# Performance work log

Hardware: AMD Instinct MI355X
Metric: run time of the kernel (lower is better)

## Reference

```python
import jax, jax.numpy as jnp
import numpy as np

N = 50000      # nodes
E = 1_600_000  # edges
FN = 8         # num_node_features
FE = 8         # num_edge_features
H = 16         # hidden_layers[0]
IH = 10        # intra_hidden


def _lin(k, i, o):
    return (jax.random.normal(k, (i, o), dtype=jnp.float32) / np.sqrt(i)).astype(jnp.float32)


def setup_inputs() -> dict:
    key = jax.random.key(0)
    ks = jax.random.split(key, 16)
    d = {}
    d["x"] = jax.random.normal(ks[0], (N, FN), dtype=jnp.float32)
    d["edge_attr"] = jax.random.normal(ks[1], (E, FE), dtype=jnp.float32)
    d["edge_index"] = jax.random.randint(ks[2], (2, E), 0, N)
    # NNConv 0: in=FN, out=H; edge-nn: FE -> IH -> FN*H
    d["c0_w1"] = _lin(ks[3], FE, IH);  d["c0_b1"] = jnp.zeros((IH,), jnp.float32)
    d["c0_w2"] = _lin(ks[4], IH, FN * H); d["c0_b2"] = jnp.zeros((FN * H,), jnp.float32)
    d["c0_root"] = _lin(ks[5], FN, H); d["c0_bias"] = jnp.zeros((H,), jnp.float32)
    # NNConv 1: in=H, out=IH; edge-nn: FE -> IH -> H*IH
    d["c1_w1"] = _lin(ks[6], FE, IH);  d["c1_b1"] = jnp.zeros((IH,), jnp.float32)
    d["c1_w2"] = _lin(ks[7], IH, H * IH); d["c1_b2"] = jnp.zeros((H * IH,), jnp.float32)
    d["c1_root"] = _lin(ks[8], H, IH); d["c1_bias"] = jnp.zeros((IH,), jnp.float32)
    # edge predictor: (FE+IH) -> IH -> 1
    d["ep_w1"] = _lin(ks[9], FE + IH, IH); d["ep_b1"] = jnp.zeros((IH,), jnp.float32)
    d["ep_w2"] = _lin(ks[10], IH, 1); d["ep_b2"] = jnp.zeros((1,), jnp.float32)
    return d


def _nnconv(x, edge_index, edge_attr, w1, b1, w2, b2, root, bias, in_ch, out_ch):
    """PyG NNConv (aggr='add', root_weight=True): per-edge weight from edge MLP,
    gather source features, per-edge matvec, scatter-add to targets, plus root term."""
    src, dst = edge_index[0], edge_index[1]
    w = jax.nn.relu(edge_attr @ w1 + b1) @ w2 + b2        # [E, in*out]
    w = w.reshape(-1, in_ch, out_ch)                       # [E, in, out]
    msg = jnp.einsum('ei,eio->eo', x[src], w)              # [E, out]
    agg = jax.ops.segment_sum(msg, dst, num_segments=x.shape[0])  # [N, out]
    return agg + x @ root + bias


def reference(x, edge_attr, edge_index,
              c0_w1, c0_b1, c0_w2, c0_b2, c0_root, c0_bias,
              c1_w1, c1_b1, c1_w2, c1_b2, c1_root, c1_bias,
              ep_w1, ep_b1, ep_w2, ep_b2):
    h = jax.nn.relu(_nnconv(x, edge_index, edge_attr,
                            c0_w1, c0_b1, c0_w2, c0_b2, c0_root, c0_bias, FN, H))
    h = jax.nn.relu(_nnconv(h, edge_index, edge_attr,
                            c1_w1, c1_b1, c1_w2, c1_b2, c1_root, c1_bias, H, IH))
    feat = jnp.concatenate([edge_attr, h[edge_index[0]]], axis=1)  # [E, FE+IH]
    scores = jax.nn.relu(feat @ ep_w1 + ep_b1) @ ep_w2 + ep_b2     # [E, 1]
    return scores.squeeze(-1)
```

## Files before the change

### kernel.cpp

```cpp
#include <hip/hip_runtime.h>

#define N_NODES 50000
#define E_EDGES 1600000
#define FN 8
#define FE 8
#define HID 16
#define IH 10
#define NB_SCAN 196

#define I_CNT   0
#define I_OFF   50048
#define I_RANK  100096
#define I_BSUM  1700096
#define I_BBASE 1700352
#define I_TOTAL 1700608
#define F_H     0
#define F_H2    800000
#define F_MSG   1300000
#define F_TOTAL 26900000
#define WS_NEED ((size_t)I_TOTAL*4 + (size_t)F_TOTAL*4)

__global__ __launch_bounds__(256) void count_rank_k(
    const int* __restrict__ ei, int* __restrict__ cnt, int* __restrict__ rank)
{
    int e = blockIdx.x * 256 + threadIdx.x;
    if (e >= E_EDGES) return;
    int dst = ei[E_EDGES + e];
    rank[e] = atomicAdd(&cnt[dst], 1);
}

__global__ __launch_bounds__(256) void blocksum_k(
    const int* __restrict__ cnt, int* __restrict__ bsum)
{
    __shared__ int sh[256];
    int t = threadIdx.x;
    int idx = blockIdx.x * 256 + t;
    sh[t] = (idx < N_NODES) ? cnt[idx] : 0;
    __syncthreads();
#pragma unroll
    for (int d = 128; d > 0; d >>= 1) {
        if (t < d) sh[t] += sh[t + d];
        __syncthreads();
    }
    if (t == 0) bsum[blockIdx.x] = sh[0];
}

__global__ __launch_bounds__(256) void scan_bsums_k(
    const int* __restrict__ bsum, int* __restrict__ bbase)
{
    __shared__ int sh[256];
    int t = threadIdx.x;
    int v = (t < NB_SCAN) ? bsum[t] : 0;
    sh[t] = v;
    __syncthreads();
#pragma unroll
    for (int d = 1; d < 256; d <<= 1) {
        int u = (t >= d) ? sh[t - d] : 0;
        __syncthreads();
        sh[t] += u;
        __syncthreads();
    }
    if (t < NB_SCAN) bbase[t] = sh[t] - v;
}

__global__ __launch_bounds__(256) void offsets_k(
    const int* __restrict__ cnt, const int* __restrict__ bbase,
    int* __restrict__ offset)
{
    __shared__ int sh[256];
    int t = threadIdx.x;
    int b = blockIdx.x;
    int idx = b * 256 + t;
    int v = (idx < N_NODES) ? cnt[idx] : 0;
    sh[t] = v;
    __syncthreads();
#pragma unroll
    for (int d = 1; d < 256; d <<= 1) {
        int u = (t >= d) ? sh[t - d] : 0;
        __syncthreads();
        sh[t] += u;
        __syncthreads();
    }
    int incl = sh[t];
    int base = bbase[b];
    if (idx < N_NODES) offset[idx] = base + incl - v;
    if (idx == N_NODES - 1) offset[N_NODES] = base + incl;
}

__device__ __forceinline__ void load8(const float* __restrict__ p, float v[8]) {
    const float4* q = reinterpret_cast<const float4*>(p);
    float4 a = q[0], b = q[1];
    v[0]=a.x; v[1]=a.y; v[2]=a.z; v[3]=a.w;
    v[4]=b.x; v[5]=b.y; v[6]=b.z; v[7]=b.w;
}

__device__ __forceinline__ void edge_mlp(
    const float eav[FE], const float* __restrict__ w1,
    const float* __restrict__ b1, float u[IH])
{
#pragma unroll
    for (int h = 0; h < IH; ++h) {
        float s = b1[h];
#pragma unroll
        for (int k = 0; k < FE; ++k) s = fmaf(eav[k], w1[k*IH + h], s);
        u[h] = fmaxf(s, 0.f);
    }
}

__global__ __launch_bounds__(256) void conv0_scatter_k(
    const float* __restrict__ x, const float* __restrict__ ea,
    const int* __restrict__ ei,
    const float* __restrict__ w1, const float* __restrict__ b1,
    const float* __restrict__ w2, const float* __restrict__ b2,
    const int* __restrict__ offset, const int* __restrict__ rank,
    float* __restrict__ msgbuf)
{
    int e = blockIdx.x * 256 + threadIdx.x;
    if (e >= E_EDGES) return;
    int src = ei[e];
    int dst = ei[E_EDGES + e];

    float eav[FE];
    load8(ea + (size_t)e * FE, eav);
    float u[IH];
    edge_mlp(eav, w1, b1, u);
    float xv[FN];
    load8(x + (size_t)src * FN, xv);

    float msg[HID];
#pragma unroll
    for (int o = 0; o < HID; ++o) msg[o] = 0.f;
#pragma unroll
    for (int i = 0; i < FN; ++i) {
        float xi = xv[i];
#pragma unroll
        for (int o = 0; o < HID; ++o) {
            float t = b2[i*HID + o];
#pragma unroll
            for (int h = 0; h < IH; ++h)
                t = fmaf(u[h], w2[h*(FN*HID) + i*HID + o], t);
            msg[o] = fmaf(xi, t, msg[o]);
        }
    }
    size_t pos = (size_t)(offset[dst] + rank[e]) * HID;
    float4* mp = reinterpret_cast<float4*>(msgbuf + pos);
    mp[0] = make_float4(msg[0],  msg[1],  msg[2],  msg[3]);
    mp[1] = make_float4(msg[4],  msg[5],  msg[6],  msg[7]);
    mp[2] = make_float4(msg[8],  msg[9],  msg[10], msg[11]);
    mp[3] = make_float4(msg[12], msg[13], msg[14], msg[15]);
}

__global__ __launch_bounds__(256) void node0_red_k(
    const float* __restrict__ x, const float* __restrict__ msgbuf,
    const int* __restrict__ offset,
    const float* __restrict__ root, const float* __restrict__ bias,
    float* __restrict__ h)
{
    int idx = blockIdx.x * 256 + threadIdx.x;
    if (idx >= N_NODES * HID) return;
    int n = idx >> 4;
    int o = idx & 15;
    int beg = offset[n], end = offset[n + 1];
    float s = bias[o];
    for (int j = beg; j < end; ++j) s += msgbuf[(size_t)j * HID + o];
    const float* xr = x + (size_t)n * FN;
#pragma unroll
    for (int i = 0; i < FN; ++i) s = fmaf(xr[i], root[i*HID + o], s);
    h[idx] = fmaxf(s, 0.f);
}

__global__ __launch_bounds__(256) void conv1_scatter_k(
    const float* __restrict__ hin, const float* __restrict__ ea,
    const int* __restrict__ ei,
    const float* __restrict__ w1, const float* __restrict__ b1,
    const float* __restrict__ w2, const float* __restrict__ b2,
    const int* __restrict__ offset, const int* __restrict__ rank,
    float* __restrict__ msgbuf)
{
    int e = blockIdx.x * 256 + threadIdx.x;
    if (e >= E_EDGES) return;
    int src = ei[e];
    int dst = ei[E_EDGES + e];

    float eav[FE];
    load8(ea + (size_t)e * FE, eav);
    float u[IH];
    edge_mlp(eav, w1, b1, u);
    float hv[HID];
    {
        const float4* p = reinterpret_cast<const float4*>(hin + (size_t)src * HID);
        float4 a = p[0], b = p[1], c = p[2], d = p[3];
        hv[0]=a.x;  hv[1]=a.y;  hv[2]=a.z;   hv[3]=a.w;
        hv[4]=b.x;  hv[5]=b.y;  hv[6]=b.z;   hv[7]=b.w;
        hv[8]=c.x;  hv[9]=c.y;  hv[10]=c.z;  hv[11]=c.w;
        hv[12]=d.x; hv[13]=d.y; hv[14]=d.z;  hv[15]=d.w;
    }
    float msg[IH];
#pragma unroll
    for (int o = 0; o < IH; ++o) msg[o] = 0.f;
#pragma unroll
    for (int i = 0; i < HID; ++i) {
        float hi = hv[i];
#pragma unroll
        for (int o = 0; o < IH; ++o) {
            float t = b2[i*IH + o];
#pragma unroll
            for (int h = 0; h < IH; ++h)
                t = fmaf(u[h], w2[h*(HID*IH) + i*IH + o], t);
            msg[o] = fmaf(hi, t, msg[o]);
        }
    }
    size_t pos = (size_t)(offset[dst] + rank[e]) * IH;
    float2* mp = reinterpret_cast<float2*>(msgbuf + pos);
    mp[0] = make_float2(msg[0], msg[1]);
    mp[1] = make_float2(msg[2], msg[3]);
    mp[2] = make_float2(msg[4], msg[5]);
    mp[3] = make_float2(msg[6], msg[7]);
    mp[4] = make_float2(msg[8], msg[9]);
}

__global__ __launch_bounds__(256) void node1_red_k(
    const float* __restrict__ hin, const float* __restrict__ msgbuf,
    const int* __restrict__ offset,
    const float* __restrict__ root, const float* __restrict__ bias,
    float* __restrict__ h2)
{
    int idx = blockIdx.x * 256 + threadIdx.x;
    if (idx >= N_NODES * IH) return;
    int n = idx / IH;
    int o = idx - n * IH;
    int beg = offset[n], end = offset[n + 1];
    float s = bias[o];
    for (int j = beg; j < end; ++j) s += msgbuf[(size_t)j * IH + o];
    const float* hr = hin + (size_t)n * HID;
#pragma unroll
    for (int i = 0; i < HID; ++i) s = fmaf(hr[i], root[i*IH + o], s);
    h2[idx] = fmaxf(s, 0.f);
}

__global__ __launch_bounds__(256) void edge_pred_k(
    const float* __restrict__ h2, const float* __restrict__ ea,
    const int* __restrict__ ei,
    const float* __restrict__ w1, const float* __restrict__ b1,
    const float* __restrict__ w2, const float* __restrict__ b2,
    float* __restrict__ out)
{
    int e = blockIdx.x * 256 + threadIdx.x;
    if (e >= E_EDGES) return;
    int src = ei[e];
    float eav[FE];
    load8(ea + (size_t)e * FE, eav);
    float hv[IH];
    {
        const float2* p = reinterpret_cast<const float2*>(h2 + (size_t)src * IH);
        float2 a = p[0], b = p[1], c = p[2], d = p[3], f = p[4];
        hv[0]=a.x; hv[1]=a.y; hv[2]=b.x; hv[3]=b.y; hv[4]=c.x;
        hv[5]=c.y; hv[6]=d.x; hv[7]=d.y; hv[8]=f.x; hv[9]=f.y;
    }
    float score = b2[0];
#pragma unroll
    for (int j = 0; j < IH; ++j) {
        float s = b1[j];
#pragma unroll
        for (int k = 0; k < FE; ++k) s = fmaf(eav[k], w1[k*IH + j], s);
#pragma unroll
        for (int k = 0; k < IH; ++k) s = fmaf(hv[k], w1[(FE + k)*IH + j], s);
        s = fmaxf(s, 0.f);
        score = fmaf(s, w2[j], score);
    }
    out[e] = score;
}

__global__ __launch_bounds__(256) void conv0_edge_k(
    const float* __restrict__ x, const float* __restrict__ ea,
    const int* __restrict__ ei,
    const float* __restrict__ w1, const float* __restrict__ b1,
    const float* __restrict__ w2, const float* __restrict__ b2,
    float* __restrict__ agg)
{
    int e = blockIdx.x * 256 + threadIdx.x;
    if (e >= E_EDGES) return;
    int src = ei[e];
    int dst = ei[E_EDGES + e];
    float eav[FE];
    load8(ea + (size_t)e * FE, eav);
    float u[IH];
    edge_mlp(eav, w1, b1, u);
    float xv[FN];
    load8(x + (size_t)src * FN, xv);
    float msg[HID];
#pragma unroll
    for (int o = 0; o < HID; ++o) msg[o] = 0.f;
#pragma unroll
    for (int i = 0; i < FN; ++i) {
        float xi = xv[i];
#pragma unroll
        for (int o = 0; o < HID; ++o) {
            float t = b2[i*HID + o];
#pragma unroll
            for (int h = 0; h < IH; ++h)
                t = fmaf(u[h], w2[h*(FN*HID) + i*HID + o], t);
            msg[o] = fmaf(xi, t, msg[o]);
        }
    }
    float* ap = agg + (size_t)dst * HID;
#pragma unroll
    for (int o = 0; o < HID; ++o) atomicAdd(ap + o, msg[o]);
}

__global__ __launch_bounds__(256) void node0_k(
    const float* __restrict__ x, const float* __restrict__ agg,
    const float* __restrict__ root, const float* __restrict__ bias,
    float* __restrict__ h)
{
    int idx = blockIdx.x * 256 + threadIdx.x;
    if (idx >= N_NODES * HID) return;
    int n = idx >> 4;
    int o = idx & 15;
    float s = agg[idx] + bias[o];
    const float* xr = x + (size_t)n * FN;
#pragma unroll
    for (int i = 0; i < FN; ++i) s = fmaf(xr[i], root[i*HID + o], s);
    h[idx] = fmaxf(s, 0.f);
}

__global__ __launch_bounds__(256) void conv1_edge_k(
    const float* __restrict__ hin, const float* __restrict__ ea,
    const int* __restrict__ ei,
    const float* __restrict__ w1, const float* __restrict__ b1,
    const float* __restrict__ w2, const float* __restrict__ b2,
    float* __restrict__ agg)
{
    int e = blockIdx.x * 256 + threadIdx.x;
    if (e >= E_EDGES) return;
    int src = ei[e];
    int dst = ei[E_EDGES + e];
    float eav[FE];
    load8(ea + (size_t)e * FE, eav);
    float u[IH];
    edge_mlp(eav, w1, b1, u);
    float hv[HID];
    {
        const float4* p = reinterpret_cast<const float4*>(hin + (size_t)src * HID);
        float4 a = p[0], b = p[1], c = p[2], d = p[3];
        hv[0]=a.x;  hv[1]=a.y;  hv[2]=a.z;   hv[3]=a.w;
        hv[4]=b.x;  hv[5]=b.y;  hv[6]=b.z;   hv[7]=b.w;
        hv[8]=c.x;  hv[9]=c.y;  hv[10]=c.z;  hv[11]=c.w;
        hv[12]=d.x; hv[13]=d.y; hv[14]=d.z;  hv[15]=d.w;
    }
    float msg[IH];
#pragma unroll
    for (int o = 0; o < IH; ++o) msg[o] = 0.f;
#pragma unroll
    for (int i = 0; i < HID; ++i) {
        float hi = hv[i];
#pragma unroll
        for (int o = 0; o < IH; ++o) {
            float t = b2[i*IH + o];
#pragma unroll
            for (int h = 0; h < IH; ++h)
                t = fmaf(u[h], w2[h*(HID*IH) + i*IH + o], t);
            msg[o] = fmaf(hi, t, msg[o]);
        }
    }
    float* ap = agg + (size_t)dst * IH;
#pragma unroll
    for (int o = 0; o < IH; ++o) atomicAdd(ap + o, msg[o]);
}

__global__ __launch_bounds__(256) void node1_k(
    const float* __restrict__ hin, const float* __restrict__ agg,
    const float* __restrict__ root, const float* __restrict__ bias,
    float* __restrict__ h2)
{
    int idx = blockIdx.x * 256 + threadIdx.x;
    if (idx >= N_NODES * IH) return;
    int n = idx / IH;
    int o = idx - n * IH;
    float s = agg[idx] + bias[o];
    const float* hr = hin + (size_t)n * HID;
#pragma unroll
    for (int i = 0; i < HID; ++i) s = fmaf(hr[i], root[i*IH + o], s);
    h2[idx] = fmaxf(s, 0.f);
}

extern "C" void kernel_launch(void* const* d_in, const int* in_sizes, int n_in,
                              void* d_out, int out_size, void* d_ws, size_t ws_size,
                              hipStream_t stream) {
    const float* x       = (const float*)d_in[0];
    const float* ea      = (const float*)d_in[1];
    const int*   ei      = (const int*)  d_in[2];
    const float* c0_w1   = (const float*)d_in[3];
    const float* c0_b1   = (const float*)d_in[4];
    const float* c0_w2   = (const float*)d_in[5];
    const float* c0_b2   = (const float*)d_in[6];
    const float* c0_root = (const float*)d_in[7];
    const float* c0_bias = (const float*)d_in[8];
    const float* c1_w1   = (const float*)d_in[9];
    const float* c1_b1   = (const float*)d_in[10];
    const float* c1_w2   = (const float*)d_in[11];
    const float* c1_b2   = (const float*)d_in[12];
    const float* c1_root = (const float*)d_in[13];
    const float* c1_bias = (const float*)d_in[14];
    const float* ep_w1   = (const float*)d_in[15];
    const float* ep_b1   = (const float*)d_in[16];
    const float* ep_w2   = (const float*)d_in[17];
    const float* ep_b2   = (const float*)d_in[18];
    float* out = (float*)d_out;

    int eb = (E_EDGES + 255) / 256;

    if (ws_size >= WS_NEED) {
        int*   wi     = (int*)d_ws;
        int*   cnt    = wi + I_CNT;
        int*   offset = wi + I_OFF;
        int*   rank   = wi + I_RANK;
        int*   bsum   = wi + I_BSUM;
        int*   bbase  = wi + I_BBASE;
        float* wf     = (float*)(wi + I_TOTAL);
        float* h      = wf + F_H;
        float* h2     = wf + F_H2;
        float* msg    = wf + F_MSG;

        hipMemsetAsync(cnt, 0, N_NODES * sizeof(int), stream);
        count_rank_k<<<eb, 256, 0, stream>>>(ei, cnt, rank);
        blocksum_k<<<NB_SCAN, 256, 0, stream>>>(cnt, bsum);
        scan_bsums_k<<<1, 256, 0, stream>>>(bsum, bbase);
        offsets_k<<<NB_SCAN, 256, 0, stream>>>(cnt, bbase, offset);

        conv0_scatter_k<<<eb, 256, 0, stream>>>(x, ea, ei, c0_w1, c0_b1, c0_w2, c0_b2,
                                                offset, rank, msg);
        node0_red_k<<<(N_NODES*HID + 255)/256, 256, 0, stream>>>(x, msg, offset,
                                                                 c0_root, c0_bias, h);
        conv1_scatter_k<<<eb, 256, 0, stream>>>(h, ea, ei, c1_w1, c1_b1, c1_w2, c1_b2,
                                                offset, rank, msg);
        node1_red_k<<<(N_NODES*IH + 255)/256, 256, 0, stream>>>(h, msg, offset,
                                                                c1_root, c1_bias, h2);
        edge_pred_k<<<eb, 256, 0, stream>>>(h2, ea, ei, ep_w1, ep_b1, ep_w2, ep_b2, out);
    } else {
        float* ws   = (float*)d_ws;
        float* agg0 = ws;
        float* agg1 = ws + 800000;
        float* h    = ws + 1300000;
        float* h2   = ws + 2100000;
        hipMemsetAsync(d_ws, 0, 1300000 * sizeof(float), stream);
        conv0_edge_k<<<eb, 256, 0, stream>>>(x, ea, ei, c0_w1, c0_b1, c0_w2, c0_b2, agg0);
        node0_k<<<(N_NODES*HID + 255)/256, 256, 0, stream>>>(x, agg0, c0_root, c0_bias, h);
        conv1_edge_k<<<eb, 256, 0, stream>>>(h, ea, ei, c1_w1, c1_b1, c1_w2, c1_b2, agg1);
        node1_k<<<(N_NODES*IH + 255)/256, 256, 0, stream>>>(h, agg1, c1_root, c1_bias, h2);
        edge_pred_k<<<eb, 256, 0, stream>>>(h2, ea, ei, ep_w1, ep_b1, ep_w2, ep_b2, out);
    }
}
```

Baseline: 303.3 us.

## Compute NNConv edge messages with bf16 MFMA over outer-product features

Both NNConv message kernels stop evaluating the per-edge weight matrices with scalar FMAs. Each edge now builds a feature row [x, u⊗x] (and [h, u⊗h] for the second layer) in shared memory, and the message comes from one bf16 16x16x32 MFMA GEMM against the reshaped w2/b2 weights. This turns roughly a thousand per-edge scalar FMAs into matrix-core work, at the cost of bf16 rounding, shared-memory staging and scattered single-float stores to the CSR-ordered buffer. Launch bounds are also changed, and the second-layer kernel moves to 128-thread blocks.

```diff
diff --git a/kernel.cpp b/kernel.cpp
--- a/kernel.cpp
+++ b/kernel.cpp
@@ -1,4 +1,5 @@
 #include <hip/hip_runtime.h>
+#include <hip/hip_bf16.h>
 
 #define N_NODES 50000
 #define E_EDGES 1600000
@@ -20,6 +21,15 @@
 #define F_TOTAL 26900000
 #define WS_NEED ((size_t)I_TOTAL*4 + (size_t)F_TOTAL*4)
 
+typedef __attribute__((ext_vector_type(8))) short bf16x8_t;
+typedef __attribute__((ext_vector_type(4))) float f32x4_t;
+
+__device__ __forceinline__ unsigned pkbf(float a, float b) {
+    union { __hip_bfloat162 v; unsigned u; } r;
+    r.v = __hip_bfloat162(__float2bfloat16(a), __float2bfloat16(b));
+    return r.u;
+}
+
 __global__ __launch_bounds__(256) void count_rank_k(
     const int* __restrict__ ei, int* __restrict__ cnt, int* __restrict__ rank)
 {
@@ -107,7 +117,7 @@
     }
 }
 
-__global__ __launch_bounds__(256) void conv0_scatter_k(
+__global__ __launch_bounds__(256, 3) void conv0_mfma_k(
     const float* __restrict__ x, const float* __restrict__ ea,
     const int* __restrict__ ei,
     const float* __restrict__ w1, const float* __restrict__ b1,
@@ -115,10 +125,34 @@
     const int* __restrict__ offset, const int* __restrict__ rank,
     float* __restrict__ msgbuf)
 {
-    int e = blockIdx.x * 256 + threadIdx.x;
-    if (e >= E_EDGES) return;
+    __shared__ alignas(16) unsigned short feat[16 * 1536];
+    __shared__ alignas(16) unsigned short bfrag[3 * 512];
+    __shared__ int posArr[256];
+
+    int t = threadIdx.x;
+    int e = blockIdx.x * 256 + t;
+
+#pragma unroll
+    for (int q = 0; q < 6; ++q) {
+        int fid = t * 6 + q;
+        int l   = (fid >> 3) & 63;
+        int j   = fid & 7;
+        int s   = fid >> 9;
+        int k   = s * 32 + ((l >> 4) << 3) + j;
+        int o   = l & 15;
+        float wv;
+        if (k < 8)        wv = b2[k * HID + o];
+        else if (k < 88)  { int kk = k - 8; wv = w2[(kk >> 3) * (FN*HID) + (kk & 7) * HID + o]; }
+        else              wv = 0.f;
+        union { __hip_bfloat16 h; unsigned short us; } cv;
+        cv.h = __float2bfloat16(wv);
+        bfrag[fid] = cv.us;
+    }
+    __syncthreads();
+
     int src = ei[e];
     int dst = ei[E_EDGES + e];
+    posArr[t] = offset[dst] + rank[e];
 
     float eav[FE];
     load8(ea + (size_t)e * FE, eav);
@@ -127,27 +161,141 @@
     float xv[FN];
     load8(x + (size_t)src * FN, xv);
 
-    float msg[HID];
-#pragma unroll
-    for (int o = 0; o < HID; ++o) msg[o] = 0.f;
-#pragma unroll
-    for (int i = 0; i < FN; ++i) {
-        float xi = xv[i];
-#pragma unroll
-        for (int o = 0; o < HID; ++o) {
-            float t = b2[i*HID + o];
-#pragma unroll
-            for (int h = 0; h < IH; ++h)
-                t = fmaf(u[h], w2[h*(FN*HID) + i*HID + o], t);
-            msg[o] = fmaf(xi, t, msg[o]);
-        }
-    }
-    size_t pos = (size_t)(offset[dst] + rank[e]) * HID;
-    float4* mp = reinterpret_cast<float4*>(msgbuf + pos);
-    mp[0] = make_float4(msg[0],  msg[1],  msg[2],  msg[3]);
-    mp[1] = make_float4(msg[4],  msg[5],  msg[6],  msg[7]);
-    mp[2] = make_float4(msg[8],  msg[9],  msg[10], msg[11]);
-    mp[3] = make_float4(msg[12], msg[13], msg[14], msg[15]);
+    int m = t >> 4, r = t & 15;
+    unsigned* fb = reinterpret_cast<unsigned*>(feat);
+#pragma unroll
+    for (int c = 0; c < 12; ++c) {
+        float v0,v1,v2,v3,v4,v5,v6,v7;
+        if (c == 0)      { v0=xv[0];v1=xv[1];v2=xv[2];v3=xv[3];v4=xv[4];v5=xv[5];v6=xv[6];v7=xv[7]; }
+        else if (c < 11) { float uh = u[c-1];
+                           v0=uh*xv[0];v1=uh*xv[1];v2=uh*xv[2];v3=uh*xv[3];
+                           v4=uh*xv[4];v5=uh*xv[5];v6=uh*xv[6];v7=uh*xv[7]; }
+        else             { v0=v1=v2=v3=v4=v5=v6=v7=0.f; }
+        int base = m*768 + (((c>>2)*64 + (c&3)*16 + r) << 2);
+        fb[base+0] = pkbf(v0,v1);
+        fb[base+1] = pkbf(v2,v3);
+        fb[base+2] = pkbf(v4,v5);
+        fb[base+3] = pkbf(v6,v7);
+    }
+
+    int lane = t & 63, wave = t >> 6;
+    bf16x8_t bfr[3];
+#pragma unroll
+    for (int s = 0; s < 3; ++s)
+        bfr[s] = *reinterpret_cast<const bf16x8_t*>(&bfrag[s*512 + lane*8]);
+
+    int col = lane & 15, rg = lane >> 4;
+#pragma unroll
+    for (int mm = 0; mm < 4; ++mm) {
+        int mt = wave * 4 + mm;
+        f32x4_t acc = {0.f, 0.f, 0.f, 0.f};
+#pragma unroll
+        for (int s = 0; s < 3; ++s) {
+            bf16x8_t af = *reinterpret_cast<const bf16x8_t*>(
+                &feat[mt*1536 + (s*64 + rg*16 + col)*8]);
+            acc = __builtin_amdgcn_mfma_f32_16x16x32_bf16(af, bfr[s], acc, 0, 0, 0);
+        }
+#pragma unroll
+        for (int j = 0; j < 4; ++j) {
+            int row = rg * 4 + j;
+            int pos = posArr[mt*16 + row];
+            msgbuf[(size_t)pos * HID + col] = acc[j];
+        }
+    }
+}
+
+__global__ __launch_bounds__(128, 2) void conv1_mfma_k(
+    const float* __restrict__ hin, const float* __restrict__ ea,
+    const int* __restrict__ ei,
+    const float* __restrict__ w1, const float* __restrict__ b1,
+    const float* __restrict__ w2, const float* __restrict__ b2,
+    const int* __restrict__ offset, const int* __restrict__ rank,
+    float* __restrict__ msgbuf)
+{
+    __shared__ alignas(16) unsigned short feat[8 * 3072];
+    __shared__ alignas(16) unsigned short bfrag[6 * 512];
+    __shared__ int posArr[128];
+
+    int t = threadIdx.x;
+    int e = blockIdx.x * 128 + t;
+
+#pragma unroll
+    for (int q = 0; q < 24; ++q) {
+        int fid = t * 24 + q;
+        int l   = (fid >> 3) & 63;
+        int j   = fid & 7;
+        int s   = fid >> 9;
+        int k   = s * 32 + ((l >> 4) << 3) + j;
+        int o   = l & 15;
+        float wv = 0.f;
+        if (o < IH) {
+            if (k < 16)        wv = b2[k * IH + o];
+            else if (k < 176)  { int kk = k - 16; wv = w2[(kk >> 4) * (HID*IH) + (kk & 15) * IH + o]; }
+        }
+        union { __hip_bfloat16 h; unsigned short us; } cv;
+        cv.h = __float2bfloat16(wv);
+        bfrag[fid] = cv.us;
+    }
+    __syncthreads();
+
+    int src = ei[e];
+    int dst = ei[E_EDGES + e];
+    posArr[t] = offset[dst] + rank[e];
+
+    float eav[FE];
+    load8(ea + (size_t)e * FE, eav);
+    float u[IH];
+    edge_mlp(eav, w1, b1, u);
+    float hv[HID];
+    load8(hin + (size_t)src * HID,     hv);
+    load8(hin + (size_t)src * HID + 8, hv + 8);
+
+    int m = t >> 4, r = t & 15;
+    unsigned* fb = reinterpret_cast<unsigned*>(feat);
+#pragma unroll
+    for (int c = 0; c < 24; ++c) {
+        float v[8];
+        if (c < 2) {
+#pragma unroll
+            for (int j = 0; j < 8; ++j) v[j] = hv[c*8 + j];
+        } else if (c < 22) {
+            float uh = u[(c - 2) >> 1];
+            int ib = ((c - 2) & 1) * 8;
+#pragma unroll
+            for (int j = 0; j < 8; ++j) v[j] = uh * hv[ib + j];
+        } else {
+#pragma unroll
+            for (int j = 0; j < 8; ++j) v[j] = 0.f;
+        }
+        int base = m*1536 + (((c>>2)*64 + (c&3)*16 + r) << 2);
+        fb[base+0] = pkbf(v[0],v[1]);
+        fb[base+1] = pkbf(v[2],v[3]);
+        fb[base+2] = pkbf(v[4],v[5]);
+        fb[base+3] = pkbf(v[6],v[7]);
+    }
+
+    int lane = t & 63, wave = t >> 6;
+    int col = lane & 15, rg = lane >> 4;
+#pragma unroll
+    for (int mm = 0; mm < 4; ++mm) {
+        int mt = wave * 4 + mm;
+        f32x4_t acc = {0.f, 0.f, 0.f, 0.f};
+#pragma unroll
+        for (int s = 0; s < 6; ++s) {
+            bf16x8_t bf = *reinterpret_cast<const bf16x8_t*>(&bfrag[s*512 + lane*8]);
+            bf16x8_t af = *reinterpret_cast<const bf16x8_t*>(
+                &feat[mt*3072 + (s*64 + rg*16 + col)*8]);
+            acc = __builtin_amdgcn_mfma_f32_16x16x32_bf16(af, bf, acc, 0, 0, 0);
+        }
+        if (col < IH) {
+#pragma unroll
+            for (int j = 0; j < 4; ++j) {
+                int row = rg * 4 + j;
+                int pos = posArr[mt*16 + row];
+                msgbuf[(size_t)pos * IH + col] = acc[j];
+            }
+        }
+    }
 }
 
 __global__ __launch_bounds__(256) void node0_red_k(
@@ -167,56 +315,6 @@
 #pragma unroll
     for (int i = 0; i < FN; ++i) s = fmaf(xr[i], root[i*HID + o], s);
     h[idx] = fmaxf(s, 0.f);
-}
-
-__global__ __launch_bounds__(256) void conv1_scatter_k(
-    const float* __restrict__ hin, const float* __restrict__ ea,
-    const int* __restrict__ ei,
-    const float* __restrict__ w1, const float* __restrict__ b1,
-    const float* __restrict__ w2, const float* __restrict__ b2,
-    const int* __restrict__ offset, const int* __restrict__ rank,
-    float* __restrict__ msgbuf)
-{
-    int e = blockIdx.x * 256 + threadIdx.x;
-    if (e >= E_EDGES) return;
-    int src = ei[e];
-    int dst = ei[E_EDGES + e];
-
-    float eav[FE];
-    load8(ea + (size_t)e * FE, eav);
-    float u[IH];
-    edge_mlp(eav, w1, b1, u);
-    float hv[HID];
-    {
-        const float4* p = reinterpret_cast<const float4*>(hin + (size_t)src * HID);
-        float4 a = p[0], b = p[1], c = p[2], d = p[3];
-        hv[0]=a.x;  hv[1]=a.y;  hv[2]=a.z;   hv[3]=a.w;
-        hv[4]=b.x;  hv[5]=b.y;  hv[6]=b.z;   hv[7]=b.w;
-        hv[8]=c.x;  hv[9]=c.y;  hv[10]=c.z;  hv[11]=c.w;
-        hv[12]=d.x; hv[13]=d.y; hv[14]=d.z;  hv[15]=d.w;
-    }
-    float msg[IH];
-#pragma unroll
-    for (int o = 0; o < IH; ++o) msg[o] = 0.f;
-#pragma unroll
-    for (int i = 0; i < HID; ++i) {
-        float hi = hv[i];
-#pragma unroll
-        for (int o = 0; o < IH; ++o) {
-            float t = b2[i*IH + o];
-#pragma unroll
-            for (int h = 0; h < IH; ++h)
-                t = fmaf(u[h], w2[h*(HID*IH) + i*IH + o], t);
-            msg[o] = fmaf(hi, t, msg[o]);
-        }
-    }
-    size_t pos = (size_t)(offset[dst] + rank[e]) * IH;
-    float2* mp = reinterpret_cast<float2*>(msgbuf + pos);
-    mp[0] = make_float2(msg[0], msg[1]);
-    mp[1] = make_float2(msg[2], msg[3]);
-    mp[2] = make_float2(msg[4], msg[5]);
-    mp[3] = make_float2(msg[6], msg[7]);
-    mp[4] = make_float2(msg[8], msg[9]);
 }
 
 __global__ __launch_bounds__(256) void node1_red_k(
@@ -340,14 +438,8 @@
     float u[IH];
     edge_mlp(eav, w1, b1, u);
     float hv[HID];
-    {
-        const float4* p = reinterpret_cast<const float4*>(hin + (size_t)src * HID);
-        float4 a = p[0], b = p[1], c = p[2], d = p[3];
-        hv[0]=a.x;  hv[1]=a.y;  hv[2]=a.z;   hv[3]=a.w;
-        hv[4]=b.x;  hv[5]=b.y;  hv[6]=b.z;   hv[7]=b.w;
-        hv[8]=c.x;  hv[9]=c.y;  hv[10]=c.z;  hv[11]=c.w;
-        hv[12]=d.x; hv[13]=d.y; hv[14]=d.z;  hv[15]=d.w;
-    }
+    load8(hin + (size_t)src * HID,     hv);
+    load8(hin + (size_t)src * HID + 8, hv + 8);
     float msg[IH];
 #pragma unroll
     for (int o = 0; o < IH; ++o) msg[o] = 0.f;
@@ -428,12 +520,12 @@
         scan_bsums_k<<<1, 256, 0, stream>>>(bsum, bbase);
         offsets_k<<<NB_SCAN, 256, 0, stream>>>(cnt, bbase, offset);
 
-        conv0_scatter_k<<<eb, 256, 0, stream>>>(x, ea, ei, c0_w1, c0_b1, c0_w2, c0_b2,
-                                                offset, rank, msg);
+        conv0_mfma_k<<<E_EDGES/256, 256, 0, stream>>>(x, ea, ei, c0_w1, c0_b1, c0_w2, c0_b2,
+                                                      offset, rank, msg);
         node0_red_k<<<(N_NODES*HID + 255)/256, 256, 0, stream>>>(x, msg, offset,
                                                                  c0_root, c0_bias, h);
-        conv1_scatter_k<<<eb, 256, 0, stream>>>(h, ea, ei, c1_w1, c1_b1, c1_w2, c1_b2,
-                                                offset, rank, msg);
+        conv1_mfma_k<<<E_EDGES/128, 128, 0, stream>>>(h, ea, ei, c1_w1, c1_b1, c1_w2, c1_b2,
+                                                      offset, rank, msg);
         node1_red_k<<<(N_NODES*IH + 255)/256, 256, 0, stream>>>(h, msg, offset,
                                                                 c1_root, c1_bias, h2);
         edge_pred_k<<<eb, 256, 0, stream>>>(h2, ea, ei, ep_w1, ep_b1, ep_w2, ep_b2, out);
```

Result: slower. 401.3 us (+32.3%).

## Split NNConv edge messages across output channels with LDS-staged weights

Applied to the files above, without the earlier changes.

Both NNConv scatter kernels stop computing a whole message per thread. Each block now stages edge MLP outputs, gathered source features and the edge-NN weights in shared memory, then spreads the output channels (and, for conv1, two input halves joined by a shuffle) across threads. Each thread keeps only its column of weights in registers, so the per-thread weight loads and the per-edge weight-matrix recompute are removed. In exchange it adds a block barrier, LDS traffic, about 90 weight registers per thread, idle lanes in conv1 (60 of 64 active), and scalar scattered stores in place of vector stores.

```diff
diff --git a/kernel.cpp b/kernel.cpp
--- a/kernel.cpp
+++ b/kernel.cpp
@@ -7,6 +7,7 @@
 #define HID 16
 #define IH 10
 #define NB_SCAN 196
+#define C1_TILE 240
 
 #define I_CNT   0
 #define I_OFF   50048
@@ -107,7 +108,7 @@
     }
 }
 
-__global__ __launch_bounds__(256) void conv0_scatter_k(
+__global__ __launch_bounds__(256) void conv0_osplit_k(
     const float* __restrict__ x, const float* __restrict__ ea,
     const int* __restrict__ ei,
     const float* __restrict__ w1, const float* __restrict__ b1,
@@ -115,39 +116,146 @@
     const int* __restrict__ offset, const int* __restrict__ rank,
     float* __restrict__ msgbuf)
 {
-    int e = blockIdx.x * 256 + threadIdx.x;
-    if (e >= E_EDGES) return;
-    int src = ei[e];
-    int dst = ei[E_EDGES + e];
-
-    float eav[FE];
-    load8(ea + (size_t)e * FE, eav);
-    float u[IH];
-    edge_mlp(eav, w1, b1, u);
-    float xv[FN];
-    load8(x + (size_t)src * FN, xv);
-
-    float msg[HID];
-#pragma unroll
-    for (int o = 0; o < HID; ++o) msg[o] = 0.f;
-#pragma unroll
-    for (int i = 0; i < FN; ++i) {
-        float xi = xv[i];
-#pragma unroll
-        for (int o = 0; o < HID; ++o) {
-            float t = b2[i*HID + o];
-#pragma unroll
-            for (int h = 0; h < IH; ++h)
-                t = fmaf(u[h], w2[h*(FN*HID) + i*HID + o], t);
-            msg[o] = fmaf(xi, t, msg[o]);
+    __shared__ float wlds[1408];
+    __shared__ float ulds[256 * 12];
+    __shared__ float xlds[256 * 8];
+    __shared__ int   plds[256];
+
+    int t = threadIdx.x;
+#pragma unroll
+    for (int q = 0; q < 6; ++q) {
+        int idx = q * 256 + t;
+        if (idx < 1408) wlds[idx] = (idx < 128) ? b2[idx] : w2[idx - 128];
+    }
+
+    int e = blockIdx.x * 256 + t;
+    {
+        int src = ei[e];
+        int dst = ei[E_EDGES + e];
+        plds[t] = offset[dst] + rank[e];
+        float eav[FE];
+        load8(ea + (size_t)e * FE, eav);
+        float u[IH];
+        edge_mlp(eav, w1, b1, u);
+        float xv[FN];
+        load8(x + (size_t)src * FN, xv);
+#pragma unroll
+        for (int i = 0; i < FN; ++i) xlds[t*8 + i] = xv[i];
+#pragma unroll
+        for (int h = 0; h < IH; ++h) ulds[t*12 + h] = u[h];
+    }
+    __syncthreads();
+
+    int o = t & 15, g = t >> 4;
+    float wb[8], ww[80];
+#pragma unroll
+    for (int i = 0; i < 8; ++i)  wb[i] = wlds[i*16 + o];
+#pragma unroll
+    for (int k = 0; k < 80; ++k) ww[k] = wlds[128 + k*16 + o];
+
+#pragma unroll 2
+    for (int j = 0; j < 16; ++j) {
+        int eidx = j * 16 + g;
+        float xv[8], uv[10];
+#pragma unroll
+        for (int i = 0; i < 8; ++i)  xv[i] = xlds[eidx*8 + i];
+#pragma unroll
+        for (int h = 0; h < 10; ++h) uv[h] = ulds[eidx*12 + h];
+        float acc = 0.f;
+#pragma unroll
+        for (int i = 0; i < 8; ++i) acc = fmaf(xv[i], wb[i], acc);
+#pragma unroll
+        for (int h = 0; h < 10; ++h) {
+            float th = 0.f;
+#pragma unroll
+            for (int i = 0; i < 8; ++i) th = fmaf(xv[i], ww[h*8 + i], th);
+            acc = fmaf(uv[h], th, acc);
         }
-    }
-    size_t pos = (size_t)(offset[dst] + rank[e]) * HID;
-    float4* mp = reinterpret_cast<float4*>(msgbuf + pos);
-    mp[0] = make_float4(msg[0],  msg[1],  msg[2],  msg[3]);
-    mp[1] = make_float4(msg[4],  msg[5],  msg[6],  msg[7]);
-    mp[2] = make_float4(msg[8],  msg[9],  msg[10], msg[11]);
-    mp[3] = make_float4(msg[12], msg[13], msg[14], msg[15]);
+        msgbuf[(size_t)plds[eidx] * HID + o] = acc;
+    }
+}
+
+__global__ __launch_bounds__(256) void conv1_osplit_k(
+    const float* __restrict__ hin, const float* __restrict__ ea,
+    const int* __restrict__ ei,
+    const float* __restrict__ w1, const float* __restrict__ b1,
+    const float* __restrict__ w2, const float* __restrict__ b2,
+    const int* __restrict__ offset, const int* __restrict__ rank,
+    float* __restrict__ msgbuf)
+{
+    __shared__ float wlds[1760];
+    __shared__ float ulds[C1_TILE * 12];
+    __shared__ float hlds[C1_TILE * 20];
+    __shared__ int   plds[C1_TILE];
+
+    int t = threadIdx.x;
+#pragma unroll
+    for (int q = 0; q < 7; ++q) {
+        int idx = q * 256 + t;
+        if (idx < 1760) wlds[idx] = (idx < 1600) ? w2[idx] : b2[idx - 1600];
+    }
+
+    int ebase = blockIdx.x * C1_TILE;
+    if (t < C1_TILE) {
+        int e = ebase + t;
+        int ee = (e < E_EDGES) ? e : 0;
+        int src = ei[ee];
+        int dst = ei[E_EDGES + ee];
+        plds[t] = offset[dst] + rank[ee];
+        float eav[FE];
+        load8(ea + (size_t)ee * FE, eav);
+        float u[IH];
+        edge_mlp(eav, w1, b1, u);
+        float hv[HID];
+        load8(hin + (size_t)src * HID,     hv);
+        load8(hin + (size_t)src * HID + 8, hv + 8);
+#pragma unroll
+        for (int i = 0; i < HID; ++i) hlds[t*20 + i] = hv[i];
+#pragma unroll
+        for (int h = 0; h < IH; ++h)  ulds[t*12 + h] = u[h];
+    }
+    __syncthreads();
+
+    int lane = t & 63, wv = t >> 6;
+    int esub = lane / 20; if (esub > 2) esub = 2;
+    int rem  = lane % 20;
+    int oo = rem % 10, ihalf = rem / 10;
+    bool active = (lane < 60);
+    int partner = active ? (ihalf == 0 ? lane + 10 : lane - 10) : lane;
+
+    float ww[80], wb[8];
+#pragma unroll
+    for (int h = 0; h < 10; ++h)
+#pragma unroll
+        for (int i = 0; i < 8; ++i)
+            ww[h*8 + i] = wlds[h*160 + (ihalf*8 + i)*10 + oo];
+#pragma unroll
+    for (int i = 0; i < 8; ++i) wb[i] = wlds[1600 + (ihalf*8 + i)*10 + oo];
+
+#pragma unroll 2
+    for (int j = 0; j < 20; ++j) {
+        int eidx = j * 12 + wv * 3 + esub;
+        float hv[8], uv[10];
+#pragma unroll
+        for (int i = 0; i < 8; ++i)  hv[i] = hlds[eidx*20 + ihalf*8 + i];
+#pragma unroll
+        for (int h = 0; h < 10; ++h) uv[h] = ulds[eidx*12 + h];
+        float acc = 0.f;
+#pragma unroll
+        for (int i = 0; i < 8; ++i) acc = fmaf(hv[i], wb[i], acc);
+#pragma unroll
+        for (int h = 0; h < 10; ++h) {
+            float th = 0.f;
+#pragma unroll
+            for (int i = 0; i < 8; ++i) th = fmaf(hv[i], ww[h*8 + i], th);
+            acc = fmaf(uv[h], th, acc);
+        }
+        float other = __shfl(acc, partner, 64);
+        float msgv = acc + other;
+        int eg = ebase + eidx;
+        if (active && ihalf == 0 && eg < E_EDGES)
+            msgbuf[(size_t)plds[eidx] * IH + oo] = msgv;
+    }
 }
 
 __global__ __launch_bounds__(256) void node0_red_k(
@@ -167,56 +275,6 @@
 #pragma unroll
     for (int i = 0; i < FN; ++i) s = fmaf(xr[i], root[i*HID + o], s);
     h[idx] = fmaxf(s, 0.f);
-}
-
-__global__ __launch_bounds__(256) void conv1_scatter_k(
-    const float* __restrict__ hin, const float* __restrict__ ea,
-    const int* __restrict__ ei,
-    const float* __restrict__ w1, const float* __restrict__ b1,
-    const float* __restrict__ w2, const float* __restrict__ b2,
-    const int* __restrict__ offset, const int* __restrict__ rank,
-    float* __restrict__ msgbuf)
-{
-    int e = blockIdx.x * 256 + threadIdx.x;
-    if (e >= E_EDGES) return;
-    int src = ei[e];
-    int dst = ei[E_EDGES + e];
-
-    float eav[FE];
-    load8(ea + (size_t)e * FE, eav);
-    float u[IH];
-    edge_mlp(eav, w1, b1, u);
-    float hv[HID];
-    {
-        const float4* p = reinterpret_cast<const float4*>(hin + (size_t)src * HID);
-        float4 a = p[0], b = p[1], c = p[2], d = p[3];
-        hv[0]=a.x;  hv[1]=a.y;  hv[2]=a.z;   hv[3]=a.w;
-        hv[4]=b.x;  hv[5]=b.y;  hv[6]=b.z;   hv[7]=b.w;
-        hv[8]=c.x;  hv[9]=c.y;  hv[10]=c.z;  hv[11]=c.w;
-        hv[12]=d.x; hv[13]=d.y; hv[14]=d.z;  hv[15]=d.w;
-    }
-    float msg[IH];
-#pragma unroll
-    for (int o = 0; o < IH; ++o) msg[o] = 0.f;
-#pragma unroll
-    for (int i = 0; i < HID; ++i) {
-        float hi = hv[i];
-#pragma unroll
-        for (int o = 0; o < IH; ++o) {
-            float t = b2[i*IH + o];
-#pragma unroll
-            for (int h = 0; h < IH; ++h)
-                t = fmaf(u[h], w2[h*(HID*IH) + i*IH + o], t);
-            msg[o] = fmaf(hi, t, msg[o]);
-        }
-    }
-    size_t pos = (size_t)(offset[dst] + rank[e]) * IH;
-    float2* mp = reinterpret_cast<float2*>(msgbuf + pos);
-    mp[0] = make_float2(msg[0], msg[1]);
-    mp[1] = make_float2(msg[2], msg[3]);
-    mp[2] = make_float2(msg[4], msg[5]);
-    mp[3] = make_float2(msg[6], msg[7]);
-    mp[4] = make_float2(msg[8], msg[9]);
 }
 
 __global__ __launch_bounds__(256) void node1_red_k(
@@ -340,14 +398,8 @@
     float u[IH];
     edge_mlp(eav, w1, b1, u);
     float hv[HID];
-    {
-        const float4* p = reinterpret_cast<const float4*>(hin + (size_t)src * HID);
-        float4 a = p[0], b = p[1], c = p[2], d = p[3];
-        hv[0]=a.x;  hv[1]=a.y;  hv[2]=a.z;   hv[3]=a.w;
-        hv[4]=b.x;  hv[5]=b.y;  hv[6]=b.z;   hv[7]=b.w;
-        hv[8]=c.x;  hv[9]=c.y;  hv[10]=c.z;  hv[11]=c.w;
-        hv[12]=d.x; hv[13]=d.y; hv[14]=d.z;  hv[15]=d.w;
-    }
+    load8(hin + (size_t)src * HID,     hv);
+    load8(hin + (size_t)src * HID + 8, hv + 8);
     float msg[IH];
 #pragma unroll
     for (int o = 0; o < IH; ++o) msg[o] = 0.f;
@@ -428,12 +480,12 @@
         scan_bsums_k<<<1, 256, 0, stream>>>(bsum, bbase);
         offsets_k<<<NB_SCAN, 256, 0, stream>>>(cnt, bbase, offset);
 
-        conv0_scatter_k<<<eb, 256, 0, stream>>>(x, ea, ei, c0_w1, c0_b1, c0_w2, c0_b2,
-                                                offset, rank, msg);
+        conv0_osplit_k<<<E_EDGES/256, 256, 0, stream>>>(x, ea, ei, c0_w1, c0_b1,
+                                                        c0_w2, c0_b2, offset, rank, msg);
         node0_red_k<<<(N_NODES*HID + 255)/256, 256, 0, stream>>>(x, msg, offset,
                                                                  c0_root, c0_bias, h);
-        conv1_scatter_k<<<eb, 256, 0, stream>>>(h, ea, ei, c1_w1, c1_b1, c1_w2, c1_b2,
-                                                offset, rank, msg);
+        conv1_osplit_k<<<(E_EDGES + C1_TILE - 1)/C1_TILE, 256, 0, stream>>>(
+            h, ea, ei, c1_w1, c1_b1, c1_w2, c1_b2, offset, rank, msg);
         node1_red_k<<<(N_NODES*IH + 255)/256, 256, 0, stream>>>(h, msg, offset,
                                                                 c1_root, c1_bias, h2);
         edge_pred_k<<<eb, 256, 0, stream>>>(h2, ea, ei, ep_w1, ep_b1, ep_w2, ep_b2, out);
```

Result: slower. 344.0 us (+13.4%).
